# Optimization experiments

Hardware: AMD Instinct MI355X
Metric: run time of the kernel (lower is better)

Reference implementation:

```python
import jax, jax.numpy as jnp
import numpy as np

B_, L, S_IN, S_OUT, Z_IN, Z_OUT = 2, 768, 1280, 32, 1, 32
D_INNER, D_STATE, D_CONV, DT_RANK = 64, 16, 4, 2  # expand=2 -> d_inner=64; dt_rank=ceil(32/16)=2


def setup_inputs() -> dict:
    key = jax.random.key(0)
    ks = jax.random.split(key, 12)
    p = lambda i, shape, scale=0.02: jax.random.normal(ks[i], shape, jnp.float32) * scale
    return dict(
        s=jax.random.normal(ks[0], (B_, L, S_IN), jnp.float32),
        z=jax.random.normal(ks[1], (B_, L, L, Z_IN), jnp.float32),
        s_proj_w=p(2, (S_OUT, S_IN)), s_proj_b=jnp.zeros((S_OUT,), jnp.float32),
        z_proj_w=p(3, (Z_OUT, Z_IN)), z_proj_b=jnp.zeros((Z_OUT,), jnp.float32),
        in_proj_w=p(4, (2 * D_INNER, S_OUT)),
        conv_w=p(5, (D_INNER, D_CONV)), conv_b=jnp.zeros((D_INNER,), jnp.float32),
        x_proj_w=p(6, (DT_RANK + 2 * D_STATE, D_INNER)),
        dt_proj_w=p(7, (D_INNER, DT_RANK)), dt_proj_b=p(8, (D_INNER,), 1.0),
        A_log=jnp.log(jnp.broadcast_to(jnp.arange(1, D_STATE + 1, dtype=jnp.float32), (D_INNER, D_STATE))),
        D=jnp.ones((D_INNER,), jnp.float32),
        out_proj_w=p(9, (S_OUT, D_INNER)),
    )


def mamba(u, in_proj_w, conv_w, conv_b, x_proj_w, dt_proj_w, dt_proj_b, A_log, D, out_proj_w):
    # u: [b, l, d_model]
    b, l, _ = u.shape
    xz = u @ in_proj_w.T                      # [b, l, 2*d_inner]
    x, gate = jnp.split(xz, 2, axis=-1)
    # causal depthwise conv1d, kernel D_CONV, then SiLU
    xp = jnp.pad(x, ((0, 0), (D_CONV - 1, 0), (0, 0)))
    x = sum(xp[:, k:k + l, :] * conv_w[:, k] for k in range(D_CONV)) + conv_b
    x = jax.nn.silu(x)
    x_dbl = x @ x_proj_w.T                    # [b, l, dt_rank + 2*d_state]
    dt, Bm, Cm = jnp.split(x_dbl, [DT_RANK, DT_RANK + D_STATE], axis=-1)
    dt = jax.nn.softplus(dt @ dt_proj_w.T + dt_proj_b)   # [b, l, d_inner]
    A = -jnp.exp(A_log)                       # [d_inner, d_state]
    dA = jnp.exp(dt[..., None] * A)           # [b, l, d, n]
    dBu = dt[..., None] * Bm[:, :, None, :] * x[..., None]  # [b, l, d, n]

    def step(h, ins):
        dA_t, dBu_t, C_t = ins
        h = dA_t * h + dBu_t                  # [b, d, n]
        return h, jnp.einsum('bdn,bn->bd', h, C_t)

    h0 = jnp.zeros((b, D_INNER, D_STATE), u.dtype)
    _, ys = jax.lax.scan(step, h0, (jnp.swapaxes(dA, 0, 1), jnp.swapaxes(dBu, 0, 1), jnp.swapaxes(Cm, 0, 1)))
    y = jnp.swapaxes(ys, 0, 1) + x * D        # D skip connection
    y = y * jax.nn.silu(gate)                 # gated output
    return y @ out_proj_w.T                   # [b, l, d_model]


def reference(s, z, s_proj_w, s_proj_b, z_proj_w, z_proj_b, in_proj_w, conv_w, conv_b,
              x_proj_w, dt_proj_w, dt_proj_b, A_log, D, out_proj_w):
    s_prime = s @ s_proj_w.T + s_proj_b                       # [b, l, 32]
    s_prime = mamba(s_prime, in_proj_w, conv_w, conv_b, x_proj_w,
                    dt_proj_w, dt_proj_b, A_log, D, out_proj_w)
    z_prime = z @ z_proj_w.T + z_proj_b                       # [b, l, l, 32]
    z_prime = z_prime + jnp.einsum('bsf,btf->bstf', s_prime, s_prime)
    return (s_prime, z_prime)
```

## Files before the change

kernel.cpp:

```cpp
#include <hip/hip_runtime.h>
#include <math.h>

#define B_     2
#define L_     768
#define SIN_   1280
#define SOUT_  32
#define DI_    64
#define DST_   16
#define DCONV_ 4
#define DTR_   2
#define NCH    48
#define CH     16


__global__ __launch_bounds__(256) void k_sproj(
    const float* __restrict__ s, const float* __restrict__ spw,
    const float* __restrict__ spb, const float* __restrict__ ipw,
    float* __restrict__ xz)
{
    __shared__ float srow[4][SIN_];
    __shared__ float w2[128 * 33];
    __shared__ float u[4][SOUT_];
    const int tid = threadIdx.x;
    const int row0 = blockIdx.x * 4;

    for (int r = 0; r < 4; ++r) {
        const float4* src = (const float4*)(s + (long)(row0 + r) * SIN_);
        for (int i = tid; i < SIN_ / 4; i += 256)
            ((float4*)srow[r])[i] = src[i];
    }
    for (int i = tid; i < 128 * 32; i += 256)
        w2[(i >> 5) * 33 + (i & 31)] = ipw[i];
    __syncthreads();

    const int f = tid >> 3;
    const int c = tid & 7;
    float p0 = 0.f, p1 = 0.f, p2 = 0.f, p3 = 0.f;
    const float* wrow = spw + (long)f * SIN_;
    for (int k = c; k < SIN_; k += 8) {
        float w = wrow[k];
        p0 += srow[0][k] * w; p1 += srow[1][k] * w;
        p2 += srow[2][k] * w; p3 += srow[3][k] * w;
    }
    #pragma unroll
    for (int m = 1; m <= 4; m <<= 1) {
        p0 += __shfl_xor(p0, m); p1 += __shfl_xor(p1, m);
        p2 += __shfl_xor(p2, m); p3 += __shfl_xor(p3, m);
    }
    if (c == 0) {
        float b = spb[f];
        u[0][f] = p0 + b; u[1][f] = p1 + b;
        u[2][f] = p2 + b; u[3][f] = p3 + b;
    }
    __syncthreads();

    const int j  = tid & 127;
    const int rh = tid >> 7;
    #pragma unroll
    for (int rp = 0; rp < 2; ++rp) {
        int r = rp * 2 + rh;
        float acc = 0.f;
        const float* wj = &w2[j * 33];
        #pragma unroll
        for (int k = 0; k < SOUT_; ++k) acc += u[r][k] * wj[k];
        xz[(long)(row0 + r) * 128 + j] = acc;
    }
}

__global__ __launch_bounds__(256) void k_pre(
    const float* __restrict__ xz, const float* __restrict__ convw,
    const float* __restrict__ convb, const float* __restrict__ xpw,
    const float* __restrict__ dtw, const float* __restrict__ dtb,
    float* __restrict__ xs_out, float* __restrict__ dtf,
    float* __restrict__ dtx, float* __restrict__ Bws, float* __restrict__ Cws)
{
    const int row0 = blockIdx.x * 4;
    const int tid = threadIdx.x;
    const int r = tid >> 6, d = tid & 63;
    const int row = row0 + r;
    const int b = row / L_, l = row - b * L_;
    __shared__ float sxpw[64][34];
    __shared__ float sdtw[128];
    __shared__ float sxs[4][DI_];
    __shared__ float sxd[4][34];

    for (int i = tid; i < 34 * 64; i += 256) {
        int j = i >> 6, k = i & 63;
        sxpw[k][j] = xpw[i];
    }
    if (tid < 128) sdtw[tid] = dtw[tid];

    float xc = convb[d];
    #pragma unroll
    for (int k = 0; k < DCONV_; ++k) {
        int ls = l + k - (DCONV_ - 1);
        if (ls >= 0) xc = fmaf(xz[(long)(b * L_ + ls) * 128 + d], convw[d * 4 + k], xc);
    }
    float xsv = xc / (1.f + expf(-xc));
    sxs[r][d] = xsv;
    xs_out[(long)row * DI_ + d] = xsv;
    __syncthreads();

    if (d < DTR_ + 2 * DST_) {
        float acc = 0.f;
        #pragma unroll
        for (int k = 0; k < 64; ++k) acc = fmaf(sxs[r][k], sxpw[k][d], acc);
        sxd[r][d] = acc;
    }
    __syncthreads();

    if (d < DST_) {
        Bws[(long)row * DST_ + d] = sxd[r][DTR_ + d];
        Cws[(long)row * DST_ + d] = sxd[r][DTR_ + DST_ + d];
    }
    float dtv = fmaf(sxd[r][0], sdtw[d * 2], fmaf(sxd[r][1], sdtw[d * 2 + 1], dtb[d]));
    dtv = dtv > 20.f ? dtv : log1pf(expf(dtv));
    dtf[(long)row * DI_ + d] = dtv;
    dtx[(long)row * DI_ + d] = dtv * xsv;
}

__global__ __launch_bounds__(256) void k_scan_p1(
    const float* __restrict__ dtf, const float* __restrict__ dtx,
    const float* __restrict__ Bws, const float* __restrict__ Alog,
    float* __restrict__ Pst, float* __restrict__ Lst)
{
    const int blk = blockIdx.x;
    const int dq  = blk & 3;
    const int bc  = blk >> 2;
    const int b   = bc / NCH, c = bc - b * NCH;
    const int tid = threadIdx.x;
    const int dl  = tid >> 4, n = tid & 15;
    const int d   = dq * 16 + dl;
    const long base = (long)b * L_ + c * CH;

    __shared__ float sB[CH][16];
    __shared__ float sdt[CH][16];
    __shared__ float sdx[CH][16];

    if (tid < 64) ((float4*)sB)[tid] = ((const float4*)(Bws + base * DST_))[tid];
    {
        int l = tid >> 4, j = tid & 15;
        sdt[l][j] = dtf[(base + l) * DI_ + dq * 16 + j];
        sdx[l][j] = dtx[(base + l) * DI_ + dq * 16 + j];
    }
    float A2 = -expf(Alog[d * DST_ + n]) * 1.44269504088896f;
    float P = 1.f, hl = 0.f;
    __syncthreads();

    #pragma unroll
    for (int l = 0; l < CH; ++l) {
        float a = exp2f(sdt[l][dl] * A2);
        P *= a;
        hl = fmaf(a, hl, sdx[l][dl] * sB[l][n]);
    }
    long o = (long)bc * 1024 + dq * 256 + tid;
    Pst[o] = P;
    Lst[o] = hl;
}

__global__ __launch_bounds__(256) void k_scan_p2(
    const float* __restrict__ Pst, const float* __restrict__ Lst,
    float* __restrict__ Hst)
{
    const int idx = blockIdx.x * 256 + threadIdx.x;
    const int b = idx >> 10, e = idx & 1023;
    float H = 0.f;
    #pragma unroll 8
    for (int c = 0; c < NCH; ++c) {
        long o = ((long)(b * NCH + c)) * 1024 + e;
        Hst[o] = H;
        H = fmaf(Pst[o], H, Lst[o]);
    }
}

__global__ __launch_bounds__(1024) void k_back(
    const float* __restrict__ dtf, const float* __restrict__ dtx,
    const float* __restrict__ Bws, const float* __restrict__ Cws,
    const float* __restrict__ Alog, const float* __restrict__ Hst,
    const float* __restrict__ xs, const float* __restrict__ xz,
    const float* __restrict__ Dv, const float* __restrict__ opw,
    float* __restrict__ sp)
{
    const int bc  = blockIdx.x;
    const int b   = bc / NCH, c = bc - b * NCH;
    const int tid = threadIdx.x;
    const long base = (long)b * L_ + c * CH;

    __shared__ float sB[CH][16], sC[CH][16];
    __shared__ float sdt[CH][64], sdx[CH][64];
    __shared__ float sy[CH][65];
    __shared__ float sw[64][33];

    if (tid < 64) {
        ((float4*)sB)[tid] = ((const float4*)(Bws + base * DST_))[tid];
        ((float4*)sC)[tid] = ((const float4*)(Cws + base * DST_))[tid];
    }
    {
        int l = tid >> 6, dd = tid & 63;
        sdt[l][dd] = dtf[(base + l) * DI_ + dd];
        sdx[l][dd] = dtx[(base + l) * DI_ + dd];
    }
    if (tid < SOUT_ * DI_) sw[tid & 63][tid >> 6] = opw[tid];

    const int d = tid >> 4, n = tid & 15;
    float A2 = -expf(Alog[d * DST_ + n]) * 1.44269504088896f;
    float h = Hst[(long)bc * 1024 + tid];
    __syncthreads();

    #pragma unroll
    for (int l = 0; l < CH; ++l) {
        float a = exp2f(sdt[l][d] * A2);
        h = fmaf(a, h, sdx[l][d] * sB[l][n]);
        float y = h * sC[l][n];
        y += __shfl_xor(y, 1);
        y += __shfl_xor(y, 2);
        y += __shfl_xor(y, 4);
        y += __shfl_xor(y, 8);
        if (n == 0) sy[l][d] = y;
    }
    __syncthreads();

    {
        int r = tid >> 6, dd = tid & 63;
        float g  = xz[(base + r) * 128 + DI_ + dd];
        float yv = fmaf(xs[(base + r) * DI_ + dd], Dv[dd], sy[r][dd]);
        sy[r][dd] = yv * (g / (1.f + expf(-g)));
    }
    __syncthreads();

    if (tid < CH * SOUT_) {
        int r = tid >> 5, o = tid & 31;
        float acc = 0.f;
        #pragma unroll
        for (int k = 0; k < DI_; ++k) acc = fmaf(sy[r][k], sw[k][o], acc);
        sp[(base + r) * SOUT_ + o] = acc;
    }
}

__global__ __launch_bounds__(256) void k_z(
    const float* __restrict__ z, const float* __restrict__ zw,
    const float* __restrict__ zb, const float* __restrict__ sp,
    float* __restrict__ zout)
{
    const int idx = blockIdx.x * 256 + threadIdx.x;
    const int bs  = idx / 6144;
    const int rem = idx - bs * 6144;
    const int t   = rem >> 3;
    const int f4  = rem & 7;
    const int b   = bs / L_;

    float zval = z[(long)bs * L_ + t];
    float4 w4 = ((const float4*)zw)[f4];
    float4 b4 = ((const float4*)zb)[f4];
    float4 ss = ((const float4*)sp)[bs * 8 + f4];
    float4 st = ((const float4*)sp)[(b * L_ + t) * 8 + f4];
    float4 o;
    o.x = zval * w4.x + b4.x + ss.x * st.x;
    o.y = zval * w4.y + b4.y + ss.y * st.y;
    o.z = zval * w4.z + b4.z + ss.z * st.z;
    o.w = zval * w4.w + b4.w + ss.w * st.w;
    ((float4*)zout)[(long)idx] = o;
}

extern "C" void kernel_launch(void* const* d_in, const int* in_sizes, int n_in,
                              void* d_out, int out_size, void* d_ws, size_t ws_size,
                              hipStream_t stream) {
    const float* s     = (const float*)d_in[0];
    const float* z     = (const float*)d_in[1];
    const float* spw   = (const float*)d_in[2];
    const float* spb   = (const float*)d_in[3];
    const float* zw    = (const float*)d_in[4];
    const float* zb    = (const float*)d_in[5];
    const float* ipw   = (const float*)d_in[6];
    const float* convw = (const float*)d_in[7];
    const float* convb = (const float*)d_in[8];
    const float* xpw   = (const float*)d_in[9];
    const float* dtw   = (const float*)d_in[10];
    const float* dtb   = (const float*)d_in[11];
    const float* Alog  = (const float*)d_in[12];
    const float* Dv    = (const float*)d_in[13];
    const float* opw   = (const float*)d_in[14];

    float* out = (float*)d_out;
    float* ws  = (float*)d_ws;
    float* xz  = ws;
    float* xs  = ws + 196608;
    float* dtf = ws + 294912;
    float* dtx = ws + 393216;
    float* Bws = ws + 491520;
    float* Cws = ws + 516096;
    float* Pst = ws + 540672;
    float* Lst = ws + 638976;
    float* Hst = ws + 737280;

    float* sp   = out;
    float* zout = out + 49152;

    k_sproj  <<<(B_ * L_) / 4, 256, 0, stream>>>(s, spw, spb, ipw, xz);
    k_pre    <<<(B_ * L_) / 4, 256, 0, stream>>>(xz, convw, convb, xpw, dtw, dtb,
                                                 xs, dtf, dtx, Bws, Cws);
    k_scan_p1<<<B_ * NCH * 4, 256, 0, stream>>>(dtf, dtx, Bws, Alog, Pst, Lst);
    k_scan_p2<<<8, 256, 0, stream>>>(Pst, Lst, Hst);
    k_back   <<<B_ * NCH, 1024, 0, stream>>>(dtf, dtx, Bws, Cws, Alog, Hst,
                                             xs, xz, Dv, opw, sp);
    k_z      <<<(B_ * L_ * L_ * 8) / 256, 256, 0, stream>>>(z, zw, zb, sp, zout);
}
```

Measured before the change: 260.8 us.

## Split scan back-pass into rescan and epilogue, vectorize projections, nontemporal z stores

The 96-block, 1024-thread back-pass is split into a 384-block rescan kernel that writes y to a workspace buffer and a separate 384-block epilogue that applies the D skip, gate and output projection. The s projection now handles two rows per block and reads with float4 loads. The pre kernel stages the conv window in shared memory and reads x_proj weights straight from global memory. The z output is written with nontemporal stores to avoid polluting caches. The aim is more parallelism in the small kernels, in exchange for one extra launch and extra workspace traffic.

```diff
diff --git a/kernel.cpp b/kernel.cpp
--- a/kernel.cpp
+++ b/kernel.cpp
@@ -12,19 +12,21 @@
 #define NCH    48
 #define CH     16
 
+typedef float nfloat4 __attribute__((ext_vector_type(4)));
+
 
 __global__ __launch_bounds__(256) void k_sproj(
     const float* __restrict__ s, const float* __restrict__ spw,
     const float* __restrict__ spb, const float* __restrict__ ipw,
     float* __restrict__ xz)
 {
-    __shared__ float srow[4][SIN_];
+    __shared__ float srow[2][SIN_];
     __shared__ float w2[128 * 33];
-    __shared__ float u[4][SOUT_];
-    const int tid = threadIdx.x;
-    const int row0 = blockIdx.x * 4;
-
-    for (int r = 0; r < 4; ++r) {
+    __shared__ float u[2][SOUT_];
+    const int tid = threadIdx.x;
+    const int row0 = blockIdx.x * 2;
+
+    for (int r = 0; r < 2; ++r) {
         const float4* src = (const float4*)(s + (long)(row0 + r) * SIN_);
         for (int i = tid; i < SIN_ / 4; i += 256)
             ((float4*)srow[r])[i] = src[i];
@@ -35,88 +37,95 @@
 
     const int f = tid >> 3;
     const int c = tid & 7;
-    float p0 = 0.f, p1 = 0.f, p2 = 0.f, p3 = 0.f;
-    const float* wrow = spw + (long)f * SIN_;
-    for (int k = c; k < SIN_; k += 8) {
-        float w = wrow[k];
-        p0 += srow[0][k] * w; p1 += srow[1][k] * w;
-        p2 += srow[2][k] * w; p3 += srow[3][k] * w;
+    float p0 = 0.f, p1 = 0.f;
+    const float4* w4p = (const float4*)(spw + (long)f * SIN_);
+    const float4* a0p = (const float4*)srow[0];
+    const float4* a1p = (const float4*)srow[1];
+    for (int k4 = c; k4 < SIN_ / 4; k4 += 8) {
+        float4 w  = w4p[k4];
+        float4 a0 = a0p[k4];
+        float4 a1 = a1p[k4];
+        p0 = fmaf(a0.x, w.x, fmaf(a0.y, w.y, fmaf(a0.z, w.z, fmaf(a0.w, w.w, p0))));
+        p1 = fmaf(a1.x, w.x, fmaf(a1.y, w.y, fmaf(a1.z, w.z, fmaf(a1.w, w.w, p1))));
     }
     #pragma unroll
     for (int m = 1; m <= 4; m <<= 1) {
-        p0 += __shfl_xor(p0, m); p1 += __shfl_xor(p1, m);
-        p2 += __shfl_xor(p2, m); p3 += __shfl_xor(p3, m);
+        p0 += __shfl_xor(p0, m);
+        p1 += __shfl_xor(p1, m);
     }
     if (c == 0) {
-        float b = spb[f];
-        u[0][f] = p0 + b; u[1][f] = p1 + b;
-        u[2][f] = p2 + b; u[3][f] = p3 + b;
-    }
-    __syncthreads();
-
-    const int j  = tid & 127;
-    const int rh = tid >> 7;
+        float bb = spb[f];
+        u[0][f] = p0 + bb;
+        u[1][f] = p1 + bb;
+    }
+    __syncthreads();
+
+    const int j = tid & 127;
+    const int r = tid >> 7;
+    float acc = 0.f;
+    const float* wj = &w2[j * 33];
     #pragma unroll
-    for (int rp = 0; rp < 2; ++rp) {
-        int r = rp * 2 + rh;
-        float acc = 0.f;
-        const float* wj = &w2[j * 33];
-        #pragma unroll
-        for (int k = 0; k < SOUT_; ++k) acc += u[r][k] * wj[k];
-        xz[(long)(row0 + r) * 128 + j] = acc;
-    }
-}
-
-__global__ __launch_bounds__(256) void k_pre(
+    for (int k = 0; k < SOUT_; ++k) acc += u[r][k] * wj[k];
+    xz[(long)(row0 + r) * 128 + j] = acc;
+}
+
+__global__ __launch_bounds__(256) void k_pre2(
     const float* __restrict__ xz, const float* __restrict__ convw,
     const float* __restrict__ convb, const float* __restrict__ xpw,
     const float* __restrict__ dtw, const float* __restrict__ dtb,
-    float* __restrict__ xs_out, float* __restrict__ dtf,
-    float* __restrict__ dtx, float* __restrict__ Bws, float* __restrict__ Cws)
+    float* __restrict__ xs_o, float* __restrict__ dtf_o,
+    float* __restrict__ dtx_o, float* __restrict__ Bws, float* __restrict__ Cws)
 {
     const int row0 = blockIdx.x * 4;
-    const int tid = threadIdx.x;
-    const int r = tid >> 6, d = tid & 63;
-    const int row = row0 + r;
-    const int b = row / L_, l = row - b * L_;
-    __shared__ float sxpw[64][34];
-    __shared__ float sdtw[128];
+    const int b = row0 / L_, l = row0 - b * L_;
+    const long rbase = (long)row0;
+    const int tid = threadIdx.x;
+
+    __shared__ float sx[7][DI_];
     __shared__ float sxs[4][DI_];
     __shared__ float sxd[4][34];
 
-    for (int i = tid; i < 34 * 64; i += 256) {
-        int j = i >> 6, k = i & 63;
-        sxpw[k][j] = xpw[i];
-    }
-    if (tid < 128) sdtw[tid] = dtw[tid];
-
-    float xc = convb[d];
-    #pragma unroll
-    for (int k = 0; k < DCONV_; ++k) {
-        int ls = l + k - (DCONV_ - 1);
-        if (ls >= 0) xc = fmaf(xz[(long)(b * L_ + ls) * 128 + d], convw[d * 4 + k], xc);
-    }
-    float xsv = xc / (1.f + expf(-xc));
-    sxs[r][d] = xsv;
-    xs_out[(long)row * DI_ + d] = xsv;
-    __syncthreads();
-
-    if (d < DTR_ + 2 * DST_) {
-        float acc = 0.f;
+    for (int i = tid; i < 7 * DI_; i += 256) {
+        int j = i >> 6, d = i & 63;
+        int ls = l - 3 + j;
+        sx[j][d] = (ls >= 0) ? xz[(long)(b * L_ + ls) * 128 + d] : 0.f;
+    }
+    __syncthreads();
+
+    {
+        int r = tid >> 6, d = tid & 63;
+        float xc = convb[d];
         #pragma unroll
-        for (int k = 0; k < 64; ++k) acc = fmaf(sxs[r][k], sxpw[k][d], acc);
-        sxd[r][d] = acc;
-    }
-    __syncthreads();
-
-    if (d < DST_) {
-        Bws[(long)row * DST_ + d] = sxd[r][DTR_ + d];
-        Cws[(long)row * DST_ + d] = sxd[r][DTR_ + DST_ + d];
-    }
-    float dtv = fmaf(sxd[r][0], sdtw[d * 2], fmaf(sxd[r][1], sdtw[d * 2 + 1], dtb[d]));
-    dtv = dtv > 20.f ? dtv : log1pf(expf(dtv));
-    dtf[(long)row * DI_ + d] = dtv;
-    dtx[(long)row * DI_ + d] = dtv * xsv;
+        for (int k = 0; k < DCONV_; ++k)
+            xc = fmaf(sx[r + k][d], convw[d * 4 + k], xc);
+        float xv = xc / (1.f + expf(-xc));
+        sxs[r][d] = xv;
+        xs_o[rbase * DI_ + tid] = xv;
+    }
+    __syncthreads();
+
+    if (tid < 4 * 34) {
+        int r = tid / 34, o = tid - r * 34;
+        const float* w = xpw + (long)o * DI_;
+        float a = 0.f;
+        #pragma unroll
+        for (int k = 0; k < DI_; ++k) a = fmaf(sxs[r][k], w[k], a);
+        sxd[r][o] = a;
+    }
+    __syncthreads();
+
+    {
+        int r = tid >> 6, d = tid & 63;
+        float dtv = fmaf(sxd[r][0], dtw[2 * d], fmaf(sxd[r][1], dtw[2 * d + 1], dtb[d]));
+        dtv = dtv > 20.f ? dtv : log1pf(expf(dtv));
+        dtf_o[rbase * DI_ + tid] = dtv;
+        dtx_o[rbase * DI_ + tid] = dtv * sxs[r][d];
+    }
+    if (tid < 128) {
+        int r = tid >> 5, j = tid & 31;
+        if (j < DST_) Bws[(rbase + r) * DST_ + j] = sxd[r][DTR_ + j];
+        else          Cws[(rbase + r) * DST_ + (j - DST_)] = sxd[r][DTR_ + j];
+    }
 }
 
 __global__ __launch_bounds__(256) void k_scan_p1(
@@ -158,7 +167,7 @@
     Lst[o] = hl;
 }
 
-__global__ __launch_bounds__(256) void k_scan_p2(
+__global__ __launch_bounds__(256) void k_carry(
     const float* __restrict__ Pst, const float* __restrict__ Lst,
     float* __restrict__ Hst)
 {
@@ -173,67 +182,77 @@
     }
 }
 
-__global__ __launch_bounds__(1024) void k_back(
+__global__ __launch_bounds__(256) void k_rescan(
     const float* __restrict__ dtf, const float* __restrict__ dtx,
     const float* __restrict__ Bws, const float* __restrict__ Cws,
     const float* __restrict__ Alog, const float* __restrict__ Hst,
-    const float* __restrict__ xs, const float* __restrict__ xz,
-    const float* __restrict__ Dv, const float* __restrict__ opw,
-    float* __restrict__ sp)
-{
-    const int bc  = blockIdx.x;
+    float* __restrict__ ysc)
+{
+    const int blk = blockIdx.x;
+    const int dq  = blk & 3;
+    const int bc  = blk >> 2;
     const int b   = bc / NCH, c = bc - b * NCH;
     const int tid = threadIdx.x;
+    const int dl  = tid >> 4, n = tid & 15;
+    const int d   = dq * 16 + dl;
     const long base = (long)b * L_ + c * CH;
 
     __shared__ float sB[CH][16], sC[CH][16];
-    __shared__ float sdt[CH][64], sdx[CH][64];
-    __shared__ float sy[CH][65];
-    __shared__ float sw[64][33];
+    __shared__ float sdt[CH][16], sdx[CH][16];
 
     if (tid < 64) {
         ((float4*)sB)[tid] = ((const float4*)(Bws + base * DST_))[tid];
         ((float4*)sC)[tid] = ((const float4*)(Cws + base * DST_))[tid];
     }
     {
-        int l = tid >> 6, dd = tid & 63;
-        sdt[l][dd] = dtf[(base + l) * DI_ + dd];
-        sdx[l][dd] = dtx[(base + l) * DI_ + dd];
-    }
-    if (tid < SOUT_ * DI_) sw[tid & 63][tid >> 6] = opw[tid];
-
-    const int d = tid >> 4, n = tid & 15;
+        int l = tid >> 4, j = tid & 15;
+        sdt[l][j] = dtf[(base + l) * DI_ + dq * 16 + j];
+        sdx[l][j] = dtx[(base + l) * DI_ + dq * 16 + j];
+    }
     float A2 = -expf(Alog[d * DST_ + n]) * 1.44269504088896f;
-    float h = Hst[(long)bc * 1024 + tid];
+    float h = Hst[(long)bc * 1024 + dq * 256 + tid];
     __syncthreads();
 
     #pragma unroll
     for (int l = 0; l < CH; ++l) {
-        float a = exp2f(sdt[l][d] * A2);
-        h = fmaf(a, h, sdx[l][d] * sB[l][n]);
+        float a = exp2f(sdt[l][dl] * A2);
+        h = fmaf(a, h, sdx[l][dl] * sB[l][n]);
         float y = h * sC[l][n];
         y += __shfl_xor(y, 1);
         y += __shfl_xor(y, 2);
         y += __shfl_xor(y, 4);
         y += __shfl_xor(y, 8);
-        if (n == 0) sy[l][d] = y;
-    }
-    __syncthreads();
-
-    {
-        int r = tid >> 6, dd = tid & 63;
-        float g  = xz[(base + r) * 128 + DI_ + dd];
-        float yv = fmaf(xs[(base + r) * DI_ + dd], Dv[dd], sy[r][dd]);
-        sy[r][dd] = yv * (g / (1.f + expf(-g)));
-    }
-    __syncthreads();
-
-    if (tid < CH * SOUT_) {
-        int r = tid >> 5, o = tid & 31;
+        if (n == 0) ysc[(base + l) * DI_ + d] = y;
+    }
+}
+
+__global__ __launch_bounds__(256) void k_epi(
+    const float* __restrict__ ysc, const float* __restrict__ xs,
+    const float* __restrict__ xz, const float* __restrict__ Dv,
+    const float* __restrict__ opw, float* __restrict__ sp)
+{
+    const int row0 = blockIdx.x * 4;
+    const int tid = threadIdx.x;
+    const int r = tid >> 6, d = tid & 63;
+    const int row = row0 + r;
+    __shared__ float sy[4][DI_];
+    __shared__ float sw[64][SOUT_];
+
+    for (int i = tid; i < SOUT_ * DI_; i += 256) {
+        int f = i >> 6, k = i & 63;
+        sw[k][f] = opw[i];
+    }
+    float g = xz[(long)row * 128 + DI_ + d];
+    float yv = fmaf(xs[(long)row * DI_ + d], Dv[d], ysc[(long)row * DI_ + d]);
+    yv *= g / (1.f + expf(-g));
+    sy[r][d] = yv;
+    __syncthreads();
+
+    if (d < SOUT_) {
         float acc = 0.f;
         #pragma unroll
-        for (int k = 0; k < DI_; ++k) acc = fmaf(sy[r][k], sw[k][o], acc);
-        sp[(base + r) * SOUT_ + o] = acc;
+        for (int k = 0; k < DI_; ++k) acc = fmaf(sy[r][k], sw[k][d], acc);
+        sp[(long)row * SOUT_ + d] = acc;
     }
 }
 
@@ -254,12 +273,12 @@
     float4 b4 = ((const float4*)zb)[f4];
     float4 ss = ((const float4*)sp)[bs * 8 + f4];
     float4 st = ((const float4*)sp)[(b * L_ + t) * 8 + f4];
-    float4 o;
+    nfloat4 o;
     o.x = zval * w4.x + b4.x + ss.x * st.x;
     o.y = zval * w4.y + b4.y + ss.y * st.y;
     o.z = zval * w4.z + b4.z + ss.z * st.z;
     o.w = zval * w4.w + b4.w + ss.w * st.w;
-    ((float4*)zout)[(long)idx] = o;
+    __builtin_nontemporal_store(o, (nfloat4*)zout + (long)idx);
 }
 
 extern "C" void kernel_launch(void* const* d_in, const int* in_sizes, int n_in,
@@ -289,19 +308,20 @@
     float* dtx = ws + 393216;
     float* Bws = ws + 491520;
     float* Cws = ws + 516096;
-    float* Pst = ws + 540672;
-    float* Lst = ws + 638976;
-    float* Hst = ws + 737280;
+    float* ysc = ws + 540672;
+    float* Pst = ws + 638976;
+    float* Lst = ws + 737280;
+    float* Hst = ws + 835584;
 
     float* sp   = out;
     float* zout = out + 49152;
 
-    k_sproj  <<<(B_ * L_) / 4, 256, 0, stream>>>(s, spw, spb, ipw, xz);
-    k_pre    <<<(B_ * L_) / 4, 256, 0, stream>>>(xz, convw, convb, xpw, dtw, dtb,
+    k_sproj  <<<(B_ * L_) / 2, 256, 0, stream>>>(s, spw, spb, ipw, xz);
+    k_pre2   <<<(B_ * L_) / 4, 256, 0, stream>>>(xz, convw, convb, xpw, dtw, dtb,
                                                  xs, dtf, dtx, Bws, Cws);
     k_scan_p1<<<B_ * NCH * 4, 256, 0, stream>>>(dtf, dtx, Bws, Alog, Pst, Lst);
-    k_scan_p2<<<8, 256, 0, stream>>>(Pst, Lst, Hst);
-    k_back   <<<B_ * NCH, 1024, 0, stream>>>(dtf, dtx, Bws, Cws, Alog, Hst,
-                                             xs, xz, Dv, opw, sp);
+    k_carry  <<<8, 256, 0, stream>>>(Pst, Lst, Hst);
+    k_rescan <<<B_ * NCH * 4, 256, 0, stream>>>(dtf, dtx, Bws, Cws, Alog, Hst, ysc);
+    k_epi    <<<(B_ * L_) / 4, 256, 0, stream>>>(ysc, xs, xz, Dv, opw, sp);
     k_z      <<<(B_ * L_ * L_ * 8) / 256, 256, 0, stream>>>(z, zw, zb, sp, zout);
 }
```

Measured after the change: 258.5 us. About the same (-0.9%).
